# Kernel tuning notes

Measured on AMD Instinct MI355X. Metric: run time of the kernel, lower is better.

The kernel has to match this reference:

```python
import jax, jax.numpy as jnp
import numpy as np

N = 100000      # nodes
E = 1600000     # nonzeros in sparse H (avg degree 16)
IN_DIM = 128
HID = 128
OUT = 128


def setup_inputs() -> dict:
    key = jax.random.key(0)
    k = jax.random.split(key, 8)
    X = jax.random.normal(k[0], (N, IN_DIM), dtype=jnp.float32)
    H_rows = jax.random.randint(k[1], (E,), 0, N, dtype=jnp.int32)
    H_cols = jax.random.randint(k[2], (E,), 0, N, dtype=jnp.int32)
    H_vals = jax.random.uniform(k[3], (E,), dtype=jnp.float32)
    # Linear params (PyTorch: y = x @ W.T + b); store as [in, out] for x @ W
    s1 = 1.0 / np.sqrt(IN_DIM)
    s2 = 1.0 / np.sqrt(HID)
    W1 = jax.random.uniform(k[4], (IN_DIM, HID), jnp.float32, -s1, s1)
    b1 = jax.random.uniform(k[5], (HID,), jnp.float32, -s1, s1)
    W2 = jax.random.uniform(k[6], (HID, OUT), jnp.float32, -s2, s2)
    b2 = jax.random.uniform(k[7], (OUT,), jnp.float32, -s2, s2)
    return {"X": X, "H_rows": H_rows, "H_cols": H_cols, "H_vals": H_vals,
            "W1": W1, "b1": b1, "W2": W2, "b2": b2}


def _spmm(rows, cols, vals, X):
    # sparse [N,N] @ dense [N,d] via edge gather + segment-sum
    msgs = vals[:, None] * X[cols]            # [E, d]
    return jax.ops.segment_sum(msgs, rows, num_segments=N)


def reference(X, H_rows, H_cols, H_vals, W1, b1, W2, b2):
    # num_layers == 2 branch; dropout is identity (eval mode)
    h = _spmm(H_rows, H_cols, H_vals, X @ W1 + b1)   # H @ W1(X)
    h = jax.nn.relu(h)
    out = _spmm(H_rows, H_cols, H_vals, h @ W2 + b2) # H @ W2(h)
    return out
```

## Files before the change

kernel.cpp:

```cpp
#include <hip/hip_runtime.h>

#define NNODES 100000
#define DIM 128
#define BROWS 256
#define NB ((NNODES + BROWS - 1) / BROWS)
#define BCAP 5120
#define CHUNK 4096

typedef _Float16 half8 __attribute__((ext_vector_type(8)));
typedef float f32x4 __attribute__((ext_vector_type(4)));
typedef unsigned int u32x4 __attribute__((ext_vector_type(4)));
typedef unsigned long long u64;

__device__ __forceinline__ unsigned int pack_bf16x2(float lo, float hi) {
    unsigned int ul = __float_as_uint(lo);
    unsigned int uh = __float_as_uint(hi);
    ul = (ul + 0x7fffu + ((ul >> 16) & 1u)) >> 16;
    uh = (uh + 0x7fffu + ((uh >> 16) & 1u)) & 0xffff0000u;
    return uh | ul;
}

__device__ __forceinline__ void unpack_bf16x8_v(u32x4 v, float* f) {
    f[0] = __uint_as_float(v.x << 16); f[1] = __uint_as_float(v.x & 0xffff0000u);
    f[2] = __uint_as_float(v.y << 16); f[3] = __uint_as_float(v.y & 0xffff0000u);
    f[4] = __uint_as_float(v.z << 16); f[5] = __uint_as_float(v.z & 0xffff0000u);
    f[6] = __uint_as_float(v.w << 16); f[7] = __uint_as_float(v.w & 0xffff0000u);
}

template <bool IN_BF16>
__device__ __forceinline__ void gemm_body(int blk, const void* __restrict__ Ain,
                                          const _Float16* __restrict__ Wt,
                                          const float* __restrict__ bias,
                                          unsigned short* __restrict__ Yb, int n) {
    const int t = threadIdx.x;
    const int l = t & 63;
    const int lr = l & 15;
    const int lg = l >> 4;
    const int r0 = blk * 128 + (t >> 6) * 32;

    half8 xf[2][4];
#pragma unroll
    for (int rt = 0; rt < 2; ++rt) {
        const int row = r0 + rt * 16 + lr;
        const bool ok = row < n;
        if (IN_BF16) {
            const u32x4* __restrict__ A16 = (const u32x4*)Ain;
#pragma unroll
            for (int ks = 0; ks < 4; ++ks) {
                u32x4 v = {0u, 0u, 0u, 0u};
                if (ok) v = A16[(size_t)row * 16 + ks * 4 + lg];
                float f[8];
                unpack_bf16x8_v(v, f);
                half8 h;
#pragma unroll
                for (int j = 0; j < 8; ++j) h[j] = (_Float16)f[j];
                xf[rt][ks] = h;
            }
        } else {
            const f32x4* __restrict__ A4 = (const f32x4*)Ain;
#pragma unroll
            for (int ks = 0; ks < 4; ++ks) {
                f32x4 v0 = {0.f, 0.f, 0.f, 0.f};
                f32x4 v1 = v0;
                if (ok) {
                    v0 = A4[(size_t)row * 32 + ks * 8 + lg * 2];
                    v1 = A4[(size_t)row * 32 + ks * 8 + lg * 2 + 1];
                }
                half8 h;
                h[0] = (_Float16)v0.x; h[1] = (_Float16)v0.y;
                h[2] = (_Float16)v0.z; h[3] = (_Float16)v0.w;
                h[4] = (_Float16)v1.x; h[5] = (_Float16)v1.y;
                h[6] = (_Float16)v1.z; h[7] = (_Float16)v1.w;
                xf[rt][ks] = h;
            }
        }
    }

    const f32x4 zero4 = {0.f, 0.f, 0.f, 0.f};
    f32x4 acc[2][8];
#pragma unroll
    for (int rt = 0; rt < 2; ++rt)
#pragma unroll
        for (int ct = 0; ct < 8; ++ct) acc[rt][ct] = zero4;

    const half8* __restrict__ Wf = (const half8*)Wt;
#pragma unroll
    for (int ct = 0; ct < 8; ++ct) {
        half8 wf[4];
#pragma unroll
        for (int ks = 0; ks < 4; ++ks)
            wf[ks] = Wf[(ct * 16 + lr) * 16 + ks * 4 + lg];
#pragma unroll
        for (int ks = 0; ks < 4; ++ks) {
            acc[0][ct] = __builtin_amdgcn_mfma_f32_16x16x32_f16(wf[ks], xf[0][ks], acc[0][ct], 0, 0, 0);
            acc[1][ct] = __builtin_amdgcn_mfma_f32_16x16x32_f16(wf[ks], xf[1][ks], acc[1][ct], 0, 0, 0);
        }
    }

#pragma unroll
    for (int ct = 0; ct < 8; ++ct) {
        const int c0 = ct * 16 + lg * 4;
        const float4 bv = *(const float4*)&bias[c0];
#pragma unroll
        for (int rt = 0; rt < 2; ++rt) {
            const int row = r0 + rt * 16 + lr;
            if (row < n) {
                f32x4 a = acc[rt][ct];
                const uint2 pv = make_uint2(pack_bf16x2(a[0] + bv.x, a[1] + bv.y),
                                            pack_bf16x2(a[2] + bv.z, a[3] + bv.w));
                *(uint2*)&Yb[(size_t)row * DIM + c0] = pv;
            }
        }
    }
}

__global__ __launch_bounds__(256) void pass1_bin(const int* __restrict__ rows,
                                                 const int* __restrict__ cols,
                                                 const float* __restrict__ vals,
                                                 int* __restrict__ bcnt,
                                                 int2* __restrict__ tmp, int nnz,
                                                 int p1_blocks,
                                                 const float* __restrict__ W1s,
                                                 const float* __restrict__ W2s,
                                                 _Float16* __restrict__ Wt1,
                                                 _Float16* __restrict__ Wt2) {
    __shared__ int hist[NB];
    __shared__ int base[NB];
    __shared__ int cur[NB];
    const int t = threadIdx.x;

    if (blockIdx.x >= (unsigned)p1_blocks) {
        const int b = blockIdx.x - p1_blocks;
        const float* __restrict__ W = (b & 4) ? W2s : W1s;
        _Float16* __restrict__ Wt = (b & 4) ? Wt2 : Wt1;
        const int base2 = (b & 3) * 4096;
        for (int i = t; i < 4096; i += 256) {
            const int e = base2 + i;
            const int k = e >> 7, c = e & 127;
            Wt[c * 128 + k] = (_Float16)W[e];
        }
        return;
    }

    const int e0 = blockIdx.x * CHUNK;
    const int e1 = min(e0 + CHUNK, nnz);

    for (int i = t; i < NB; i += 256) { hist[i] = 0; cur[i] = 0; }
    __syncthreads();

    for (int i = e0 + t; i < e1; i += 256)
        atomicAdd(&hist[rows[i] >> 8], 1);
    __syncthreads();

    for (int i = t; i < NB; i += 256)
        base[i] = (hist[i] > 0) ? atomicAdd(&bcnt[i], hist[i]) : 0;
    __syncthreads();

    for (int i = e0 + t; i < e1; i += 256) {
        const int r = rows[i];
        const int b = r >> 8;
        const int pos = base[b] + atomicAdd(&cur[b], 1);
        if (pos < BCAP)
            tmp[(size_t)b * BCAP + pos] =
                make_int2(((r & 255) << 24) | cols[i], __float_as_int(vals[i]));
    }
}

__global__ __launch_bounds__(256) void pass2_gemm1(const int2* __restrict__ tmp,
                                                   const int* __restrict__ bcnt,
                                                   int2* __restrict__ epack,
                                                   int* __restrict__ row_ptr,
                                                   int* __restrict__ counts,
                                                   const float* __restrict__ X,
                                                   const _Float16* __restrict__ Wt1,
                                                   const float* __restrict__ b1,
                                                   unsigned short* __restrict__ Yb, int n) {
    __shared__ int cnt[256];
    __shared__ int s[256];
    __shared__ int cur[256];

    if (blockIdx.x >= NB) {
        gemm_body<false>(blockIdx.x - NB, X, Wt1, b1, Yb, n);
        return;
    }

    const int b = blockIdx.x;
    const int t = threadIdx.x;
    const int row0 = b * BROWS;
    const int nrows = min(BROWS, n - row0);
    const int m = min(bcnt[b], BCAP);
    const int2* __restrict__ src = tmp + (size_t)b * BCAP;

    int partial = 0;
    for (int i = t; i < b; i += 256) partial += bcnt[i];
    s[t] = partial;
    __syncthreads();
    for (int off = 128; off >= 1; off >>= 1) {
        if (t < off) s[t] += s[t + off];
        __syncthreads();
    }
    const int base = s[0];
    __syncthreads();

    cnt[t] = 0;
    __syncthreads();
    for (int i = t; i < m; i += 256)
        atomicAdd(&cnt[((unsigned)src[i].x) >> 24], 1);
    __syncthreads();

    const int v = cnt[t];
    s[t] = v;
    __syncthreads();
    for (int off = 1; off < 256; off <<= 1) {
        int x = (t >= off) ? s[t - off] : 0;
        __syncthreads();
        s[t] += x;
        __syncthreads();
    }
    const int excl = s[t] - v;
    if (t < nrows) {
        row_ptr[row0 + t] = base + excl;
        counts[row0 + t] = v;
    }
    cur[t] = base + excl;
    __syncthreads();

    for (int i = t; i < m; i += 256) {
        const int2 e = src[i];
        const int rl = ((unsigned)e.x) >> 24;
        const int pos = atomicAdd(&cur[rl], 1);
        epack[pos] = make_int2(e.x & 0xFFFFFF, e.y);
    }
}

__global__ __launch_bounds__(256) void spmm1_gemm2(const int* __restrict__ row_ptr,
                                                   const int* __restrict__ counts,
                                                   const int2* __restrict__ epack,
                                                   const unsigned short* __restrict__ Xb,
                                                   const _Float16* __restrict__ Wt2,
                                                   const float* __restrict__ bias,
                                                   unsigned short* __restrict__ Yb2, int n) {
    __shared__ _Float16 hl[16][136];
    const int t = threadIdx.x;
    const int rloc = t >> 4;
    const int lane = t & 15;
    const int r = blockIdx.x * 16 + rloc;
    const bool valid = r < n;

    float acc[8];
#pragma unroll
    for (int k = 0; k < 8; ++k) acc[k] = 0.f;

    if (valid) {
        const int start = row_ptr[r];
        const int cnt = counts[r];
        const u32x4* __restrict__ X16 = (const u32x4*)Xb;
        const u64* __restrict__ ep = (const u64*)(epack + start);

        int j = 0;
        for (; j + 8 <= cnt; j += 8) {
            u64 e[8];
#pragma unroll
            for (int q = 0; q < 8; ++q) e[q] = ep[j + q];
            u32x4 x[8];
#pragma unroll
            for (int q = 0; q < 8; ++q)
                x[q] = X16[(size_t)(unsigned)(e[q] & 0xffffffffu) * 16 + lane];
#pragma unroll
            for (int q = 0; q < 8; ++q) {
                const float v = __uint_as_float((unsigned)(e[q] >> 32));
                float f[8];
                unpack_bf16x8_v(x[q], f);
#pragma unroll
                for (int k = 0; k < 8; ++k) acc[k] = fmaf(v, f[k], acc[k]);
            }
        }
        for (; j + 2 <= cnt; j += 2) {
            const u64 e0 = ep[j], e1 = ep[j + 1];
            const u32x4 x0 = X16[(size_t)(unsigned)(e0 & 0xffffffffu) * 16 + lane];
            const u32x4 x1 = X16[(size_t)(unsigned)(e1 & 0xffffffffu) * 16 + lane];
            const float v0 = __uint_as_float((unsigned)(e0 >> 32));
            const float v1 = __uint_as_float((unsigned)(e1 >> 32));
            float f0[8], f1[8];
            unpack_bf16x8_v(x0, f0); unpack_bf16x8_v(x1, f1);
#pragma unroll
            for (int k = 0; k < 8; ++k)
                acc[k] += v0 * f0[k] + v1 * f1[k];
        }
        if (j < cnt) {
            const u64 e = ep[j];
            const u32x4 x = X16[(size_t)(unsigned)(e & 0xffffffffu) * 16 + lane];
            const float v = __uint_as_float((unsigned)(e >> 32));
            float f[8];
            unpack_bf16x8_v(x, f);
#pragma unroll
            for (int k = 0; k < 8; ++k) acc[k] = fmaf(v, f[k], acc[k]);
        }
    }

    {
        half8 h;
#pragma unroll
        for (int k = 0; k < 8; ++k) h[k] = (_Float16)fmaxf(acc[k], 0.f);
        *(half8*)&hl[rloc][lane * 8] = h;
    }
    __syncthreads();

    const int l = t & 63;
    const int lr = l & 15;
    const int lg = l >> 4;
    const int w = t >> 6;

    half8 hf[4];
#pragma unroll
    for (int ks = 0; ks < 4; ++ks)
        hf[ks] = *(const half8*)&hl[lr][ks * 32 + lg * 8];

    const half8* __restrict__ Wf = (const half8*)Wt2;
    const f32x4 zero4 = {0.f, 0.f, 0.f, 0.f};
#pragma unroll
    for (int ct2 = 0; ct2 < 2; ++ct2) {
        const int ct = w * 2 + ct2;
        f32x4 a2 = zero4;
#pragma unroll
        for (int ks = 0; ks < 4; ++ks) {
            const half8 wf = Wf[(ct * 16 + lr) * 16 + ks * 4 + lg];
            a2 = __builtin_amdgcn_mfma_f32_16x16x32_f16(wf, hf[ks], a2, 0, 0, 0);
        }
        const int c0 = ct * 16 + lg * 4;
        const float4 bv = *(const float4*)&bias[c0];
        const int row = blockIdx.x * 16 + lr;
        if (row < n) {
            const uint2 pv = make_uint2(pack_bf16x2(a2[0] + bv.x, a2[1] + bv.y),
                                        pack_bf16x2(a2[2] + bv.z, a2[3] + bv.w));
            *(uint2*)&Yb2[(size_t)row * DIM + c0] = pv;
        }
    }
}

__global__ __launch_bounds__(256) void spmm_csr(const int* __restrict__ row_ptr,
                                                const int* __restrict__ counts,
                                                const int2* __restrict__ epack,
                                                const unsigned short* __restrict__ Xb,
                                                float* __restrict__ out, int n) {
    const int gid = blockIdx.x * blockDim.x + threadIdx.x;
    const int r = gid >> 4;
    const int lane = gid & 15;
    if (r >= n) return;
    const int start = row_ptr[r];
    const int cnt = counts[r];
    const u32x4* __restrict__ X16 = (const u32x4*)Xb;
    const u64* __restrict__ ep = (const u64*)(epack + start);

    float acc[8];
#pragma unroll
    for (int k = 0; k < 8; ++k) acc[k] = 0.f;

    int j = 0;
    for (; j + 8 <= cnt; j += 8) {
        u64 e[8];
#pragma unroll
        for (int q = 0; q < 8; ++q) e[q] = ep[j + q];
        u32x4 x[8];
#pragma unroll
        for (int q = 0; q < 8; ++q)
            x[q] = X16[(size_t)(unsigned)(e[q] & 0xffffffffu) * 16 + lane];
#pragma unroll
        for (int q = 0; q < 8; ++q) {
            const float v = __uint_as_float((unsigned)(e[q] >> 32));
            float f[8];
            unpack_bf16x8_v(x[q], f);
#pragma unroll
            for (int k = 0; k < 8; ++k) acc[k] = fmaf(v, f[k], acc[k]);
        }
    }
    for (; j + 2 <= cnt; j += 2) {
        const u64 e0 = ep[j], e1 = ep[j + 1];
        const u32x4 x0 = X16[(size_t)(unsigned)(e0 & 0xffffffffu) * 16 + lane];
        const u32x4 x1 = X16[(size_t)(unsigned)(e1 & 0xffffffffu) * 16 + lane];
        const float v0 = __uint_as_float((unsigned)(e0 >> 32));
        const float v1 = __uint_as_float((unsigned)(e1 >> 32));
        float f0[8], f1[8];
        unpack_bf16x8_v(x0, f0); unpack_bf16x8_v(x1, f1);
#pragma unroll
        for (int k = 0; k < 8; ++k)
            acc[k] += v0 * f0[k] + v1 * f1[k];
    }
    if (j < cnt) {
        const u64 e = ep[j];
        const u32x4 x = X16[(size_t)(unsigned)(e & 0xffffffffu) * 16 + lane];
        const float v = __uint_as_float((unsigned)(e >> 32));
        float f[8];
        unpack_bf16x8_v(x, f);
#pragma unroll
        for (int k = 0; k < 8; ++k) acc[k] = fmaf(v, f[k], acc[k]);
    }

    f32x4 a0 = {acc[0], acc[1], acc[2], acc[3]};
    f32x4 a1 = {acc[4], acc[5], acc[6], acc[7]};
    __builtin_nontemporal_store(a0, (f32x4*)&out[(size_t)r * DIM + lane * 8]);
    __builtin_nontemporal_store(a1, (f32x4*)&out[(size_t)r * DIM + lane * 8 + 4]);
}

extern "C" void kernel_launch(void* const* d_in, const int* in_sizes, int n_in,
                              void* d_out, int out_size, void* d_ws, size_t ws_size,
                              hipStream_t stream) {
    const float* X      = (const float*)d_in[0];
    const int*   H_rows = (const int*)d_in[1];
    const int*   H_cols = (const int*)d_in[2];
    const float* H_vals = (const float*)d_in[3];
    const float* W1     = (const float*)d_in[4];
    const float* b1     = (const float*)d_in[5];
    const float* W2     = (const float*)d_in[6];
    const float* b2     = (const float*)d_in[7];
    float* out = (float*)d_out;

    const int E = in_sizes[1];
    const int N = NNODES;
    const size_t bmat_bytes = (size_t)N * DIM * 2;

    const int gemm_blocks = (N + 127) / 128;
    const int p1_blocks = (E + CHUNK - 1) / CHUNK;
    const int fused_blocks = (N + 15) / 16;
    const int spmm_blocks = (N * 16 + 255) / 256;

    char* p = (char*)d_ws;
    unsigned short* Yb  = (unsigned short*)p; p += bmat_bytes;
    unsigned short* Yb2 = (unsigned short*)p; p += bmat_bytes;
    _Float16* Wt1      = (_Float16*)p;        p += 128 * 128 * 2;
    _Float16* Wt2      = (_Float16*)p;        p += 128 * 128 * 2;
    int2* epack        = (int2*)p;            p += (size_t)E * 8;
    int2* tmp          = (int2*)p;            p += (size_t)NB * BCAP * 8;
    int*  bcnt         = (int*)p;             p += (size_t)NB * 4;
    int*  row_ptr      = (int*)p;             p += (size_t)N * 4;
    int*  counts       = (int*)p;             p += (size_t)N * 4;

    hipMemsetAsync(bcnt, 0, (size_t)NB * 4, stream);
    pass1_bin<<<p1_blocks + 8, 256, 0, stream>>>(H_rows, H_cols, H_vals, bcnt, tmp, E,
                                                 p1_blocks, W1, W2, Wt1, Wt2);

    pass2_gemm1<<<NB + gemm_blocks, 256, 0, stream>>>(tmp, bcnt, epack, row_ptr, counts,
                                                      X, Wt1, b1, Yb, N);

    spmm1_gemm2<<<fused_blocks, 256, 0, stream>>>(row_ptr, counts, epack, Yb, Wt2, b2, Yb2, N);

    spmm_csr<<<spmm_blocks, 256, 0, stream>>>(row_ptr, counts, epack, Yb2, out, N);
}
```

Measured before the change: 340.1 us.

## Give each wave its own 16 rows in fused SpMM+GEMM, dropping block barrier

The fused SpMM1+GEMM2 kernel is reorganised so that each 64-lane wave owns 16 rows, with 4 lanes per row each accumulating 32 features, and each block now covers 64 rows. Because every wave writes and reads only its own LDS slice, the block-wide __syncthreads is replaced by a wave-local LDS wait, and each wave computes all 8 output column tiles itself. The intent is to remove the cross-wave barrier and give each lane more independent gather loads in flight. In exchange each lane holds 32 accumulators, which raises register pressure, and the 8-edge unrolled loop is removed, so fewer edges are batched per iteration.

```diff
diff --git a/kernel.cpp b/kernel.cpp
--- a/kernel.cpp
+++ b/kernel.cpp
@@ -240,88 +240,80 @@
                                                    const _Float16* __restrict__ Wt2,
                                                    const float* __restrict__ bias,
                                                    unsigned short* __restrict__ Yb2, int n) {
-    __shared__ _Float16 hl[16][136];
+    __shared__ _Float16 hl[4][16][136];
     const int t = threadIdx.x;
-    const int rloc = t >> 4;
-    const int lane = t & 15;
-    const int r = blockIdx.x * 16 + rloc;
-    const bool valid = r < n;
-
-    float acc[8];
-#pragma unroll
-    for (int k = 0; k < 8; ++k) acc[k] = 0.f;
-
-    if (valid) {
+    const int w = t >> 6;
+    const int l = t & 63;
+    const int rloc = l >> 2;
+    const int q = l & 3;
+    const int rbase = blockIdx.x * 64 + w * 16;
+    const int r = rbase + rloc;
+
+    float acc[32];
+#pragma unroll
+    for (int k = 0; k < 32; ++k) acc[k] = 0.f;
+
+    if (r < n) {
         const int start = row_ptr[r];
         const int cnt = counts[r];
         const u32x4* __restrict__ X16 = (const u32x4*)Xb;
         const u64* __restrict__ ep = (const u64*)(epack + start);
-
         int j = 0;
-        for (; j + 8 <= cnt; j += 8) {
-            u64 e[8];
-#pragma unroll
-            for (int q = 0; q < 8; ++q) e[q] = ep[j + q];
-            u32x4 x[8];
-#pragma unroll
-            for (int q = 0; q < 8; ++q)
-                x[q] = X16[(size_t)(unsigned)(e[q] & 0xffffffffu) * 16 + lane];
-#pragma unroll
-            for (int q = 0; q < 8; ++q) {
-                const float v = __uint_as_float((unsigned)(e[q] >> 32));
-                float f[8];
-                unpack_bf16x8_v(x[q], f);
-#pragma unroll
-                for (int k = 0; k < 8; ++k) acc[k] = fmaf(v, f[k], acc[k]);
-            }
-        }
         for (; j + 2 <= cnt; j += 2) {
             const u64 e0 = ep[j], e1 = ep[j + 1];
-            const u32x4 x0 = X16[(size_t)(unsigned)(e0 & 0xffffffffu) * 16 + lane];
-            const u32x4 x1 = X16[(size_t)(unsigned)(e1 & 0xffffffffu) * 16 + lane];
+            const size_t b0 = (size_t)(unsigned)(e0 & 0xffffffffu) * 16 + q;
+            const size_t b1 = (size_t)(unsigned)(e1 & 0xffffffffu) * 16 + q;
+            u32x4 x0[4], x1[4];
+#pragma unroll
+            for (int p2 = 0; p2 < 4; ++p2) { x0[p2] = X16[b0 + p2 * 4]; x1[p2] = X16[b1 + p2 * 4]; }
             const float v0 = __uint_as_float((unsigned)(e0 >> 32));
             const float v1 = __uint_as_float((unsigned)(e1 >> 32));
-            float f0[8], f1[8];
-            unpack_bf16x8_v(x0, f0); unpack_bf16x8_v(x1, f1);
-#pragma unroll
-            for (int k = 0; k < 8; ++k)
-                acc[k] += v0 * f0[k] + v1 * f1[k];
+#pragma unroll
+            for (int p2 = 0; p2 < 4; ++p2) {
+                float f0[8], f1[8];
+                unpack_bf16x8_v(x0[p2], f0); unpack_bf16x8_v(x1[p2], f1);
+#pragma unroll
+                for (int k = 0; k < 8; ++k)
+                    acc[p2 * 8 + k] += v0 * f0[k] + v1 * f1[k];
+            }
         }
         if (j < cnt) {
             const u64 e = ep[j];
-            const u32x4 x = X16[(size_t)(unsigned)(e & 0xffffffffu) * 16 + lane];
+            const size_t b0 = (size_t)(unsigned)(e & 0xffffffffu) * 16 + q;
             const float v = __uint_as_float((unsigned)(e >> 32));
-            float f[8];
-            unpack_bf16x8_v(x, f);
-#pragma unroll
-            for (int k = 0; k < 8; ++k) acc[k] = fmaf(v, f[k], acc[k]);
-        }
-    }
-
-    {
+#pragma unroll
+            for (int p2 = 0; p2 < 4; ++p2) {
+                const u32x4 x = X16[b0 + p2 * 4];
+                float f[8];
+                unpack_bf16x8_v(x, f);
+#pragma unroll
+                for (int k = 0; k < 8; ++k) acc[p2 * 8 + k] = fmaf(v, f[k], acc[p2 * 8 + k]);
+            }
+        }
+    }
+
+#pragma unroll
+    for (int p2 = 0; p2 < 4; ++p2) {
         half8 h;
 #pragma unroll
-        for (int k = 0; k < 8; ++k) h[k] = (_Float16)fmaxf(acc[k], 0.f);
-        *(half8*)&hl[rloc][lane * 8] = h;
-    }
-    __syncthreads();
-
-    const int l = t & 63;
+        for (int k = 0; k < 8; ++k) h[k] = (_Float16)fmaxf(acc[p2 * 8 + k], 0.f);
+        *(half8*)&hl[w][rloc][p2 * 32 + q * 8] = h;
+    }
+    asm volatile("s_waitcnt lgkmcnt(0)" ::: "memory");
+    __builtin_amdgcn_sched_barrier(0);
+
     const int lr = l & 15;
     const int lg = l >> 4;
-    const int w = t >> 6;
-
     half8 hf[4];
 #pragma unroll
     for (int ks = 0; ks < 4; ++ks)
-        hf[ks] = *(const half8*)&hl[lr][ks * 32 + lg * 8];
+        hf[ks] = *(const half8*)&hl[w][lr][ks * 32 + lg * 8];
 
     const half8* __restrict__ Wf = (const half8*)Wt2;
-    const f32x4 zero4 = {0.f, 0.f, 0.f, 0.f};
-#pragma unroll
-    for (int ct2 = 0; ct2 < 2; ++ct2) {
-        const int ct = w * 2 + ct2;
-        f32x4 a2 = zero4;
+    const int orow = rbase + lr;
+#pragma unroll
+    for (int ct = 0; ct < 8; ++ct) {
+        f32x4 a2 = {0.f, 0.f, 0.f, 0.f};
 #pragma unroll
         for (int ks = 0; ks < 4; ++ks) {
             const half8 wf = Wf[(ct * 16 + lr) * 16 + ks * 4 + lg];
@@ -329,11 +321,10 @@
         }
         const int c0 = ct * 16 + lg * 4;
         const float4 bv = *(const float4*)&bias[c0];
-        const int row = blockIdx.x * 16 + lr;
-        if (row < n) {
+        if (orow < n) {
             const uint2 pv = make_uint2(pack_bf16x2(a2[0] + bv.x, a2[1] + bv.y),
                                         pack_bf16x2(a2[2] + bv.z, a2[3] + bv.w));
-            *(uint2*)&Yb2[(size_t)row * DIM + c0] = pv;
+            *(uint2*)&Yb2[(size_t)orow * DIM + c0] = pv;
         }
     }
 }
@@ -421,7 +412,7 @@
 
     const int gemm_blocks = (N + 127) / 128;
     const int p1_blocks = (E + CHUNK - 1) / CHUNK;
-    const int fused_blocks = (N + 15) / 16;
+    const int fused_blocks = (N + 63) / 64;
     const int spmm_blocks = (N * 16 + 255) / 256;
 
     char* p = (char*)d_ws;
```

Measured after the change: 347.8 us. 1.02x slower.

## Sort rows by degree within each 256-row bin to balance SpMM wavefronts

Applied to the files above, without the earlier changes.

Adds a per-bin counting sort of rows by degree (capped at 63) in pass2, producing a permutation array. Both SpMM kernels then process rows in permuted order, so rows of similar degree share a wavefront and divergent loop trip counts are reduced. This costs an extra indirection load per row, a few more block-wide syncs in pass2, and less locality in the output and Yb2 writes.

```diff
diff --git a/kernel.cpp b/kernel.cpp
--- a/kernel.cpp
+++ b/kernel.cpp
@@ -171,6 +171,7 @@
                                                    int2* __restrict__ epack,
                                                    int* __restrict__ row_ptr,
                                                    int* __restrict__ counts,
+                                                   int* __restrict__ perm,
                                                    const float* __restrict__ X,
                                                    const _Float16* __restrict__ Wt1,
                                                    const float* __restrict__ b1,
@@ -231,11 +232,30 @@
         const int pos = atomicAdd(&cur[rl], 1);
         epack[pos] = make_int2(e.x & 0xFFFFFF, e.y);
     }
+    __syncthreads();
+
+    const int deg = (v < 63) ? v : 63;
+    if (t < 64) cur[t] = 0;
+    __syncthreads();
+    if (t < nrows) atomicAdd(&cur[deg], 1);
+    __syncthreads();
+    if (t == 0) {
+        int acc = 0;
+        for (int d = 0; d < 64; ++d) { s[d] = acc; acc += cur[d]; }
+    }
+    __syncthreads();
+    if (t < 64) cur[t] = 0;
+    __syncthreads();
+    if (t < nrows) {
+        const int pos = s[deg] + atomicAdd(&cur[deg], 1);
+        perm[row0 + pos] = row0 + t;
+    }
 }
 
 __global__ __launch_bounds__(256) void spmm1_gemm2(const int* __restrict__ row_ptr,
                                                    const int* __restrict__ counts,
                                                    const int2* __restrict__ epack,
+                                                   const int* __restrict__ perm,
                                                    const unsigned short* __restrict__ Xb,
                                                    const _Float16* __restrict__ Wt2,
                                                    const float* __restrict__ bias,
@@ -244,8 +264,9 @@
     const int t = threadIdx.x;
     const int rloc = t >> 4;
     const int lane = t & 15;
-    const int r = blockIdx.x * 16 + rloc;
-    const bool valid = r < n;
+    const int rs = blockIdx.x * 16 + rloc;
+    const bool valid = rs < n;
+    const int r = valid ? perm[rs] : 0;
 
     float acc[8];
 #pragma unroll
@@ -317,11 +338,12 @@
         hf[ks] = *(const half8*)&hl[lr][ks * 32 + lg * 8];
 
     const half8* __restrict__ Wf = (const half8*)Wt2;
-    const f32x4 zero4 = {0.f, 0.f, 0.f, 0.f};
+    const int ors = blockIdx.x * 16 + lr;
+    const int orow = (ors < n) ? perm[ors] : 0;
 #pragma unroll
     for (int ct2 = 0; ct2 < 2; ++ct2) {
         const int ct = w * 2 + ct2;
-        f32x4 a2 = zero4;
+        f32x4 a2 = {0.f, 0.f, 0.f, 0.f};
 #pragma unroll
         for (int ks = 0; ks < 4; ++ks) {
             const half8 wf = Wf[(ct * 16 + lr) * 16 + ks * 4 + lg];
@@ -329,11 +351,10 @@
         }
         const int c0 = ct * 16 + lg * 4;
         const float4 bv = *(const float4*)&bias[c0];
-        const int row = blockIdx.x * 16 + lr;
-        if (row < n) {
+        if (ors < n) {
             const uint2 pv = make_uint2(pack_bf16x2(a2[0] + bv.x, a2[1] + bv.y),
                                         pack_bf16x2(a2[2] + bv.z, a2[3] + bv.w));
-            *(uint2*)&Yb2[(size_t)row * DIM + c0] = pv;
+            *(uint2*)&Yb2[(size_t)orow * DIM + c0] = pv;
         }
     }
 }
@@ -341,12 +362,14 @@
 __global__ __launch_bounds__(256) void spmm_csr(const int* __restrict__ row_ptr,
                                                 const int* __restrict__ counts,
                                                 const int2* __restrict__ epack,
+                                                const int* __restrict__ perm,
                                                 const unsigned short* __restrict__ Xb,
                                                 float* __restrict__ out, int n) {
     const int gid = blockIdx.x * blockDim.x + threadIdx.x;
-    const int r = gid >> 4;
+    const int rs = gid >> 4;
     const int lane = gid & 15;
-    if (r >= n) return;
+    if (rs >= n) return;
+    const int r = perm[rs];
     const int start = row_ptr[r];
     const int cnt = counts[r];
     const u32x4* __restrict__ X16 = (const u32x4*)Xb;
@@ -434,15 +457,17 @@
     int*  bcnt         = (int*)p;             p += (size_t)NB * 4;
     int*  row_ptr      = (int*)p;             p += (size_t)N * 4;
     int*  counts       = (int*)p;             p += (size_t)N * 4;
+    int*  perm         = (int*)p;             p += (size_t)N * 4;
 
     hipMemsetAsync(bcnt, 0, (size_t)NB * 4, stream);
     pass1_bin<<<p1_blocks + 8, 256, 0, stream>>>(H_rows, H_cols, H_vals, bcnt, tmp, E,
                                                  p1_blocks, W1, W2, Wt1, Wt2);
 
     pass2_gemm1<<<NB + gemm_blocks, 256, 0, stream>>>(tmp, bcnt, epack, row_ptr, counts,
-                                                      X, Wt1, b1, Yb, N);
-
-    spmm1_gemm2<<<fused_blocks, 256, 0, stream>>>(row_ptr, counts, epack, Yb, Wt2, b2, Yb2, N);
-
-    spmm_csr<<<spmm_blocks, 256, 0, stream>>>(row_ptr, counts, epack, Yb2, out, N);
-}
+                                                      perm, X, Wt1, b1, Yb, N);
+
+    spmm1_gemm2<<<fused_blocks, 256, 0, stream>>>(row_ptr, counts, epack, perm,
+                                                  Yb, Wt2, b2, Yb2, N);
+
+    spmm_csr<<<spmm_blocks, 256, 0, stream>>>(row_ptr, counts, epack, perm, Yb2, out, N);
+}
```

Result: slower. 355.5 us (+4.5%).
